# Optimization experiments

Hardware: AMD Instinct MI355X
Metric: run time of the kernel (lower is better)

## Reference

```python
import jax, jax.numpy as jnp
import numpy as np

F, P, H, HEADS, C, NCLS = 18, 128, 256, 8, 32, 625
SCALES = (2, 4, 6)
MAX_ITER = 2  # self.max_iterations in the source


def _mhsa(x, Wq, bq, Wk, bk, Wv, bv, Wo, bo):
    # x: [B, S, H]. Adjacency mask is all-ones in the source (adjacency()
    # returns torch.ones), so the mask is a mathematical no-op and is omitted.
    B, S, _ = x.shape
    hd = H // HEADS
    q = (x @ Wq + bq).reshape(B, S, HEADS, hd)
    k = (x @ Wk + bk).reshape(B, S, HEADS, hd)
    v = (x @ Wv + bv).reshape(B, S, HEADS, hd)
    scores = jnp.einsum('bqhd,bkhd->bhqk', q, k) / jnp.sqrt(jnp.float32(hd))
    attn = jax.nn.softmax(scores, axis=-1)
    out = jnp.einsum('bhqk,bkhd->bqhd', attn, v).reshape(B, S, H)
    return out @ Wo + bo


def _temporal_locality(scale, emb, Wq, bq, Wk, bk, Wv, bv, Wo, bo):
    # Vectorized overlap-add version of the python loop over windows.
    nw = F - scale + 1
    idx = jnp.arange(nw)[:, None] + jnp.arange(scale)[None, :]   # [nw, scale]
    windows = emb[idx].reshape(nw, scale * P, H)                 # [nw, s*P, H]
    out = _mhsa(windows, Wq, bq, Wk, bk, Wv, bv, Wo, bo)
    out = out.reshape(nw * scale, P, H)
    gval = jnp.zeros((F, P, H), emb.dtype).at[idx.reshape(-1)].add(out)
    # overlap counts == the hardcoded norm_scale vectors for F=18
    counts = jnp.zeros((F,), emb.dtype).at[idx.reshape(-1)].add(1.0)
    return gval / counts[:, None, None]


def _forward(multiscale_embed, unary_W, unary_b, halt_W, halt_b, compat,
             mp_W, mp_b, cls_W, cls_b,
             mhsa_Wq, mhsa_bq, mhsa_Wk, mhsa_bk,
             mhsa_Wv, mhsa_bv, mhsa_Wo, mhsa_bo):
    context = jnp.zeros_like(multiscale_embed)                 # [F, P, H]
    ptn = jnp.zeros((F,), multiscale_embed.dtype)
    Rt = jnp.zeros_like(ptn)
    Nt = jnp.zeros_like(ptn)
    # unary potentials: [F, P, C] -> permute -> [P, F, C]
    marginal = (multiscale_embed @ unary_W + unary_b).transpose(1, 0, 2)
    inputs = multiscale_embed                                   # [F, P, H]
    for _ in range(MAX_ITER):
        # --- halting probability (ACT-style) ---
        p = jnp.mean(jax.nn.sigmoid(inputs @ halt_W + halt_b), axis=1)[:, 0]  # [F]
        run = (ptn < 1.0).astype(ptn.dtype)
        new_halted = (ptn + p * run > 0.99).astype(ptn.dtype) * run
        run = (ptn + p * run <= 0.99).astype(ptn.dtype) * run
        ptn = ptn + p * run
        Rt = Rt + new_halted * (1.0 - ptn)
        ptn = ptn + new_halted * Rt
        Nt = Nt + run + new_halted
        # --- message passing: multi-scale windowed self-attention ---
        g = jnp.zeros_like(inputs)
        for i, s in enumerate(SCALES):
            g = g + _temporal_locality(s, inputs,
                                       mhsa_Wq[i], mhsa_bq[i], mhsa_Wk[i], mhsa_bk[i],
                                       mhsa_Wv[i], mhsa_bv[i], mhsa_Wo[i], mhsa_bo[i])
        temporal = 0.25 * g                                     # [F, P, H]
        inputs_p = temporal.transpose(1, 0, 2)                  # [P, F, H]
        pairwise = inputs_p @ mp_W + mp_b                       # [P, F, C]
        # compatibility transform: the chunk/cat reshuffle is an identity
        # permutation; the math is out_k = sum_c compat[k,c] * pairwise[...,c]
        pairwise = jnp.einsum('pfc,kc->pfk', pairwise, compat)
        marginal = marginal - pairwise
        # --- transition function ---
        w = (p * run + new_halted * Rt)[:, None, None]          # [F,1,1]
        inputs = inputs_p.transpose(1, 0, 2)                    # [F, P, H]
        context = inputs * w + context * (1.0 - w)
    # --- cluster features ---
    # chunk/cat flattening uses index order p*F + f on both tensors
    m = jax.nn.softmax(marginal, axis=2).reshape(P * F, C)
    ctx = context.transpose(1, 0, 2).reshape(P * F, H)
    cluster_features = m.T @ ctx                                # [C, H]
    classes = jnp.sum(cluster_features, axis=0, keepdims=True) @ cls_W + cls_b
    return classes                                              # [1, NCLS]


def setup_inputs() -> dict:
    key = jax.random.key(0)
    ks = jax.random.split(key, 16)
    init = lambda k, shape: jax.random.normal(k, shape, dtype=jnp.float32) * 0.02
    return {
        'multiscale_embed': jax.random.normal(ks[0], (F, P, H), dtype=jnp.float32),
        'unary_W': init(ks[1], (H, C)),
        'unary_b': jnp.zeros((C,), jnp.float32),
        'halt_W': init(ks[2], (H, 1)),
        'halt_b': jnp.ones((1,), jnp.float32),  # bias filled with 1.0 in source
        'compat': -jnp.eye(C, dtype=jnp.float32),
        'mp_W': init(ks[3], (H, C)),
        'mp_b': jnp.zeros((C,), jnp.float32),
        'cls_W': init(ks[4], (H, NCLS)),
        'cls_b': jnp.zeros((NCLS,), jnp.float32),
        'mhsa_Wq': init(ks[5], (3, H, H)),
        'mhsa_bq': jnp.zeros((3, H), jnp.float32),
        'mhsa_Wk': init(ks[6], (3, H, H)),
        'mhsa_bk': jnp.zeros((3, H), jnp.float32),
        'mhsa_Wv': init(ks[7], (3, H, H)),
        'mhsa_bv': jnp.zeros((3, H), jnp.float32),
        'mhsa_Wo': init(ks[8], (3, H, H)),
        'mhsa_bo': jnp.zeros((3, H), jnp.float32),
        'labels': jax.random.randint(ks[9], (1,), 0, NCLS),
    }


def reference(multiscale_embed, unary_W, unary_b, halt_W, halt_b, compat,
              mp_W, mp_b, cls_W, cls_b,
              mhsa_Wq, mhsa_bq, mhsa_Wk, mhsa_bk,
              mhsa_Wv, mhsa_bv, mhsa_Wo, mhsa_bo, labels):
    del labels  # labels are not used in the forward math shown in the source
    return _forward(multiscale_embed, unary_W, unary_b, halt_W, halt_b, compat,
                    mp_W, mp_b, cls_W, cls_b,
                    mhsa_Wq, mhsa_bq, mhsa_Wk, mhsa_bk,
                    mhsa_Wv, mhsa_bv, mhsa_Wo, mhsa_bo)
```

## Files before the change

### kernel.cpp

```cpp
#include <hip/hip_runtime.h>
#include <hip/hip_bf16.h>

typedef __hip_bfloat16 bf16;

#define F 18
#define P 128
#define H 256
#define HEADS 8
#define HD 32
#define NCLS 625
#define FPH (F*P*H)
#define RPS 589824
#define NT16 144

#define OF_PTN    16
#define OF_RT     48
#define OF_W      80
#define OF_OSUM   128
#define OF_CTX    512
#define OF_FW     (OF_CTX + FPH)
#define WO2_HALTW 0
#define WO2_HALTB 256
#define WO2_CLSB  272
#define WO2_CLSW  912
#define WO2_BQ    160912
#define WO2_BK    161680
#define WO2_BV    162448
#define WO2_BO    163216
#define FW_TOTAL  163984
#define NF_TOTAL  (OF_FW + FW_TOTAL)

#define BB_WQT 0
#define BB_WKT 196608
#define BB_WVT 393216
#define BB_WOT 589824
#define BB_INP 786432
#define BB_QB  1376256
#define BB_KB  (BB_QB + 3*RPS)
#define BB_VT  (BB_KB + 3*RPS)
#define BB_AO  (BB_VT + 3*RPS)

typedef __attribute__((ext_vector_type(8))) short s8v;
typedef __attribute__((ext_vector_type(4))) short s4v;
typedef __attribute__((ext_vector_type(4))) float f4v;

__device__ __forceinline__ float b2f(bf16 x){ return __bfloat162float(x); }
__device__ __forceinline__ unsigned short f2bu(float x){
    union { __hip_bfloat16 h; unsigned short u; } cv; cv.h = __float2bfloat16(x); return cv.u;
}
__device__ __forceinline__ float bu2f(unsigned short u){
    union { unsigned int x; float f; } cv; cv.x = ((unsigned int)u) << 16; return cv.f;
}
__device__ __forceinline__ void b2x2(unsigned int u, float& a, float& b){
    union { unsigned int x; float f; } c1, c2;
    c1.x = u << 16; c2.x = u & 0xffff0000u; a = c1.f; b = c2.f;
}

#if __has_builtin(__builtin_amdgcn_cvt_pk_bf16_f32)
typedef __attribute__((ext_vector_type(2))) __bf16 bf2_t;
__device__ __forceinline__ unsigned int pk2(float a, float b){
    union { bf2_t v; unsigned int u; } cv;
    cv.v = __builtin_amdgcn_cvt_pk_bf16_f32(a, b);
    return cv.u;
}
#else
__device__ __forceinline__ unsigned int pk2(float a, float b){
    return (unsigned int)f2bu(a) | ((unsigned int)f2bu(b) << 16);
}
#endif

#if __has_builtin(__builtin_amdgcn_exp2f)
__device__ __forceinline__ float fexp2(float x){ return __builtin_amdgcn_exp2f(x); }
#else
__device__ __forceinline__ float fexp2(float x){ return exp2f(x); }
#endif

__device__ __forceinline__ int imin(int a,int b){ return a<b?a:b; }
__device__ __forceinline__ int imax(int a,int b){ return a>b?a:b; }

__device__ __forceinline__ int detect_bf16_block(const unsigned int* __restrict__ embw,
                                                 int* scnt)
{
    if (threadIdx.x == 0) *scnt = 0;
    __syncthreads();
    int c = 0;
    {
        unsigned int e = (embw[2*threadIdx.x] >> 7) & 0xffu;
        if (e >= 120u && e <= 130u) c++;
        e = (embw[2*threadIdx.x + 1] >> 7) & 0xffu;
        if (e >= 120u && e <= 130u) c++;
    }
    atomicAdd(scnt, c);
    __syncthreads();
    return (*scnt > 256) ? 1 : 0;
}

struct ConvArgs {
    const void* src[13];
    int mode[13];
    int n[13];
    int off[13];
};
__global__ __launch_bounds__(256) void k_convert(ConvArgs a,
        const unsigned int* __restrict__ embw,
        float* __restrict__ ws, bf16* __restrict__ bb)
{
    __shared__ int scnt;
    const int isbf = detect_bf16_block(embw, &scnt);
    int gid = blockIdx.x*256 + threadIdx.x;
#pragma unroll
    for (int t = 0; t < 13; ++t){
        if (gid < a.n[t]){
            float v = isbf ? b2f(((const bf16*)a.src[t])[gid])
                           : ((const float*)a.src[t])[gid];
            if (a.mode[t] == 0){
                ws[a.off[t] + gid] = v;
            } else if (a.mode[t] == 1){
                const int i = gid >> 16, rem = gid & 65535;
                const int k = rem >> 8, nn = rem & 255;
                bb[a.off[t] + (i << 16) + (nn << 8) + k] = __float2bfloat16(v);
            } else {
                bb[BB_INP + gid] = __float2bfloat16(v);
            }
            return;
        }
        gid -= a.n[t];
    }
}

__global__ __launch_bounds__(256) void k_qkv_mfma(const bf16* __restrict__ X,
        const bf16* __restrict__ WQT, const bf16* __restrict__ WKT,
        const bf16* __restrict__ WVT, const float* __restrict__ fw,
        bf16* __restrict__ qball, bf16* __restrict__ kball, bf16* __restrict__ vball)
{
    const int tid = threadIdx.x;
    if (blockIdx.z == 3){
        if (blockIdx.x >= F || blockIdx.y != 0) return;
        __shared__ float hw[H];
        __shared__ float red[256];
        float* ws = (float*)fw - OF_FW;
        const float* hW = fw + WO2_HALTW;
        const int f = blockIdx.x;
        hw[tid] = hW[tid];
        __syncthreads();
        float sg = 0.f;
        if (tid < P){
            const uint4* row = (const uint4*)(X + (size_t)(f*P + tid)*H);
            float acc = fw[WO2_HALTB];
#pragma unroll
            for (int i = 0; i < 16; ++i){
                const uint4 u = row[i];
                float a0,a1,a2,a3,a4,a5,a6,a7;
                b2x2(u.x,a0,a1); b2x2(u.y,a2,a3); b2x2(u.z,a4,a5); b2x2(u.w,a6,a7);
                const int b = i*16;
                acc = fmaf(a0,hw[b+0],acc); acc = fmaf(a1,hw[b+1],acc);
                acc = fmaf(a2,hw[b+2],acc); acc = fmaf(a3,hw[b+3],acc);
                acc = fmaf(a4,hw[b+4],acc); acc = fmaf(a5,hw[b+5],acc);
                acc = fmaf(a6,hw[b+6],acc); acc = fmaf(a7,hw[b+7],acc);
            }
            sg = 1.f/(1.f + __expf(-acc));
        }
        red[tid] = sg;
        __syncthreads();
        for (int s = 128; s > 0; s >>= 1){ if (tid < s) red[tid] += red[tid+s]; __syncthreads(); }
        if (tid == 0){
            float pf = red[0] * (1.f/P);
            float pt = ws[OF_PTN + f], rt = ws[OF_RT + f];
            float run  = (pt < 1.f) ? 1.f : 0.f;
            float cond = (pt + pf*run > 0.99f) ? 1.f : 0.f;
            float nh   = cond*run;
            run = (1.f - cond)*run;
            pt += pf*run;
            rt += nh*(1.f - pt);
            pt += nh*rt;
            ws[OF_PTN + f] = pt; ws[OF_RT + f] = rt;
            ws[OF_W   + f] = pf*run + nh*rt;
        }
        return;
    }
    const int wave = tid >> 6, lane = tid & 63;
    const int lq = lane & 15, quad = lane >> 4;
    const int m0 = blockIdx.x * 64;
    const int n0 = blockIdx.y * 64 + wave * 16;
    const int i  = blockIdx.z;
    const int wo = i << 16;

    const bf16* arow[4];
#pragma unroll
    for (int mt = 0; mt < 4; ++mt)
        arow[mt] = X + (size_t)(m0 + mt*16 + lq)*H + quad*8;
    const bf16* bqp = WQT + wo + (size_t)(n0 + lq)*H + quad*8;
    const bf16* bkp = WKT + wo + (size_t)(n0 + lq)*H + quad*8;
    const bf16* bvp = WVT + wo + (size_t)(n0 + lq)*H + quad*8;

    f4v aq[4], ak[4], av[4];
#pragma unroll
    for (int mt = 0; mt < 4; ++mt){
        aq[mt] = (f4v){0.f,0.f,0.f,0.f};
        ak[mt] = (f4v){0.f,0.f,0.f,0.f};
        av[mt] = (f4v){0.f,0.f,0.f,0.f};
    }
#pragma unroll
    for (int k0 = 0; k0 < H; k0 += 32){
        const s8v bfq = *(const s8v*)(bqp + k0);
        const s8v bfk = *(const s8v*)(bkp + k0);
        const s8v bfv = *(const s8v*)(bvp + k0);
#pragma unroll
        for (int mt = 0; mt < 4; ++mt){
            const s8v af = *(const s8v*)(arow[mt] + k0);
            aq[mt] = __builtin_amdgcn_mfma_f32_16x16x32_bf16(bfq, af, aq[mt], 0, 0, 0);
            ak[mt] = __builtin_amdgcn_mfma_f32_16x16x32_bf16(bfk, af, ak[mt], 0, 0, 0);
            av[mt] = __builtin_amdgcn_mfma_f32_16x16x32_bf16(af, bfv, av[mt], 0, 0, 0);
        }
    }
    bf16* qo = qball + (size_t)i*RPS;
    bf16* ko = kball + (size_t)i*RPS;
    bf16* vo = vball + (size_t)i*RPS;

    const int cbase = n0 + 4*quad;
    const float4 bq4 = *(const float4*)(fw + WO2_BQ + i*256 + cbase);
    const float4 bk4 = *(const float4*)(fw + WO2_BK + i*256 + cbase);
    const int h2q  = cbase >> 5;
    const int dimq = (cbase >> 3) & 3;
    const int j2b  = cbase & 7;
    const int colv = n0 + lq;
    const float bvv = fw[WO2_BV + i*256 + colv];
    const int h2v = colv >> 5;
    const int half = (colv >> 4) & 1;
    const int lqv  = colv & 15;
#pragma unroll
    for (int mt = 0; mt < 4; ++mt){
        const int t16 = (m0 >> 4) + mt;
        const size_t qkidx = ((size_t)(h2q*NT16 + t16)*64 + lq + 16*dimq)*8 + j2b;
        uint2 qst, kst;
        qst.x = pk2(aq[mt][0] + bq4.x, aq[mt][1] + bq4.y);
        qst.y = pk2(aq[mt][2] + bq4.z, aq[mt][3] + bq4.w);
        kst.x = pk2(ak[mt][0] + bk4.x, ak[mt][1] + bk4.y);
        kst.y = pk2(ak[mt][2] + bk4.z, ak[mt][3] + bk4.w);
        *(uint2*)(qo + qkidx) = qst;
        *(uint2*)(ko + qkidx) = kst;
        const size_t vbase = ((size_t)(h2v*NT16 + t16)*64 + lqv + 16*quad)*8 + half*4;
        uint2 vst;
        vst.x = pk2(av[mt][0] + bvv, av[mt][1] + bvv);
        vst.y = pk2(av[mt][2] + bvv, av[mt][3] + bvv);
        *(uint2*)(vo + vbase) = vst;
    }
}

#if __has_builtin(__builtin_amdgcn_mfma_f32_16x16x16bf16_1k)
#define ATTN_HAVE_1K 1
#else
#define ATTN_HAVE_1K 0
#endif

template<int SS>
__device__ __forceinline__ void attn_body(const bf16* __restrict__ qs,
        const bf16* __restrict__ ks, const bf16* __restrict__ vs,
        bf16* __restrict__ aos, int f, int h, int t, int lane)
{
    const int NW = F - SS + 1;
    const int lq = lane & 15, quad = lane >> 4;
    const int qt16 = f*8 + t;

    s8v qf;
    {
        const float SCL2 = 0.17677669529663687f * 1.4426950408889634f;
        union { s8v v; unsigned int u[4]; } qin, qsc;
        qin.v = *(const s8v*)(qs + ((size_t)(h*NT16 + qt16)*64 + lane)*8);
#pragma unroll
        for (int j = 0; j < 4; ++j){
            float a, b;
            b2x2(qin.u[j], a, b);
            qsc.u[j] = pk2(a*SCL2, b*SCL2);
        }
        qf = qsc.v;
    }

    const int wLo = imax(0, f - SS + 1);
    const int wHi = imin(NW - 1, f);
    const int cnt = wHi - wLo + 1;
    const int gHi = wHi + SS - 1;

    float mw[SS], lw[SS];
    f4v ow0[SS], ow1[SS];
#pragma unroll
    for (int ws = 0; ws < SS; ++ws){
        mw[ws] = -3e38f; lw[ws] = 0.f;
        ow0[ws] = (f4v){0.f,0.f,0.f,0.f};
        ow1[ws] = (f4v){0.f,0.f,0.f,0.f};
    }

    for (int g = wLo; g <= gHi; ++g){
        const int kt0 = g*8;
        f4v st[8];
#pragma unroll
        for (int tt = 0; tt < 4; ++tt){
            const s8v kf0 = *(const s8v*)(ks + ((size_t)(h*NT16 + kt0 + tt*2    )*64 + lane)*8);
            const s8v kf1 = *(const s8v*)(ks + ((size_t)(h*NT16 + kt0 + tt*2 + 1)*64 + lane)*8);
            f4v z = {0.f,0.f,0.f,0.f};
            st[2*tt]   = __builtin_amdgcn_mfma_f32_16x16x32_bf16(kf0, qf, z, 0, 0, 0);
            st[2*tt+1] = __builtin_amdgcn_mfma_f32_16x16x32_bf16(kf1, qf, z, 0, 0, 0);
        }
        union { uint4 q; s4v h2v[2]; } vA[4], vB[4];
#pragma unroll
        for (int tt = 0; tt < 4; ++tt){
            vA[tt].q = *(const uint4*)(vs + ((size_t)(h*NT16 + kt0 + tt*2    )*64 + lane)*8);
            vB[tt].q = *(const uint4*)(vs + ((size_t)(h*NT16 + kt0 + tt*2 + 1)*64 + lane)*8);
        }
        float mu = -3e38f;
#pragma unroll
        for (int t8 = 0; t8 < 8; ++t8)
            mu = fmaxf(mu, fmaxf(fmaxf(st[t8][0], st[t8][1]), fmaxf(st[t8][2], st[t8][3])));
        mu = fmaxf(mu, __shfl_xor(mu, 16));
        mu = fmaxf(mu, __shfl_xor(mu, 32));
        float Lg = 0.f;
#pragma unroll
        for (int t8 = 0; t8 < 8; ++t8){
#pragma unroll
            for (int r = 0; r < 4; ++r){
                const float e = fexp2(st[t8][r] - mu);
                st[t8][r] = e;
                Lg += e;
            }
        }
        Lg += __shfl_xor(Lg, 16);
        Lg += __shfl_xor(Lg, 32);
        f4v P0 = {0.f,0.f,0.f,0.f}, P1 = {0.f,0.f,0.f,0.f};
#pragma unroll
        for (int tt = 0; tt < 4; ++tt){
#if ATTN_HAVE_1K
            union { unsigned int u[2]; s4v v; } pf0, pf1;
            pf0.u[0] = pk2(st[2*tt][0],   st[2*tt][1]);
            pf0.u[1] = pk2(st[2*tt][2],   st[2*tt][3]);
            pf1.u[0] = pk2(st[2*tt+1][0], st[2*tt+1][1]);
            pf1.u[1] = pk2(st[2*tt+1][2], st[2*tt+1][3]);
            P0 = __builtin_amdgcn_mfma_f32_16x16x16bf16_1k(vA[tt].h2v[0], pf0.v, P0, 0, 0, 0);
            P0 = __builtin_amdgcn_mfma_f32_16x16x16bf16_1k(vB[tt].h2v[0], pf1.v, P0, 0, 0, 0);
            P1 = __builtin_amdgcn_mfma_f32_16x16x16bf16_1k(vA[tt].h2v[1], pf0.v, P1, 0, 0, 0);
            P1 = __builtin_amdgcn_mfma_f32_16x16x16bf16_1k(vB[tt].h2v[1], pf1.v, P1, 0, 0, 0);
#else
            union { s4v h2v[2]; s8v v; } va0, va1;
            va0.h2v[0] = vA[tt].h2v[0]; va0.h2v[1] = vB[tt].h2v[0];
            va1.h2v[0] = vA[tt].h2v[1]; va1.h2v[1] = vB[tt].h2v[1];
            const unsigned int p0x = pk2(st[2*tt][0],   st[2*tt][1]);
            const unsigned int p0y = pk2(st[2*tt][2],   st[2*tt][3]);
            const unsigned int p1x = pk2(st[2*tt+1][0], st[2*tt+1][1]);
            const unsigned int p1y = pk2(st[2*tt+1][2], st[2*tt+1][3]);
            const int srcA = lq + ((( quad<<1)      & 3) << 4);
            const int srcB = lq + ((((quad<<1) | 1) & 3) << 4);
            const unsigned int a0 = (unsigned int)__shfl((int)p0x, srcA);
            const unsigned int a1 = (unsigned int)__shfl((int)p0y, srcA);
            const unsigned int a2 = (unsigned int)__shfl((int)p0x, srcB);
            const unsigned int a3 = (unsigned int)__shfl((int)p0y, srcB);
            const unsigned int b0 = (unsigned int)__shfl((int)p1x, srcA);
            const unsigned int b1 = (unsigned int)__shfl((int)p1y, srcA);
            const unsigned int b2 = (unsigned int)__shfl((int)p1x, srcB);
            const unsigned int b3 = (unsigned int)__shfl((int)p1y, srcB);
            const bool hi = (quad >= 2);
            union { unsigned int u[4]; s8v v; } bfr;
            bfr.u[0] = hi ? b0 : a0; bfr.u[1] = hi ? b1 : a1;
            bfr.u[2] = hi ? b2 : a2; bfr.u[3] = hi ? b3 : a3;
            P0 = __builtin_amdgcn_mfma_f32_16x16x32_bf16(va0.v, bfr.v, P0, 0, 0, 0);
            P1 = __builtin_amdgcn_mfma_f32_16x16x32_bf16(va1.v, bfr.v, P1, 0, 0, 0);
#endif
        }
#pragma unroll
        for (int ws = 0; ws < SS; ++ws){
            const int w = wLo + ws;
            if (w <= wHi && w <= g && w >= g - SS + 1){
                const float mn = fmaxf(mw[ws], mu);
                const float a = fexp2(mw[ws] - mn);
                const float b = fexp2(mu - mn);
                lw[ws] = lw[ws]*a + Lg*b;
#pragma unroll
                for (int r = 0; r < 4; ++r){
                    ow0[ws][r] = ow0[ws][r]*a + P0[r]*b;
                    ow1[ws][r] = ow1[ws][r]*a + P1[r]*b;
                }
                mw[ws] = mn;
            }
        }
    }
    f4v acc0 = {0.f,0.f,0.f,0.f}, acc1 = {0.f,0.f,0.f,0.f};
#pragma unroll
    for (int ws = 0; ws < SS; ++ws){
        if (ws < cnt){
            const float inv = 1.f / (lw[ws] * (float)cnt);
#pragma unroll
            for (int r = 0; r < 4; ++r){
                acc0[r] += ow0[ws][r]*inv;
                acc1[r] += ow1[ws][r]*inv;
            }
        }
    }
    const int grp0 = (4*h + (quad >> 1)) & 3;
    const int grp1 = (4*h + 2 + (quad >> 1)) & 3;
    const int off  = 4*(quad & 1);
    const size_t base = (size_t)(qt16*8 + h)*64;
    uint2 s0, s1;
    s0.x = pk2(acc0[0], acc0[1]); s0.y = pk2(acc0[2], acc0[3]);
    s1.x = pk2(acc1[0], acc1[1]); s1.y = pk2(acc1[2], acc1[3]);
    *(uint2*)(aos + (base + lq + 16*grp0)*8 + off) = s0;
    *(uint2*)(aos + (base + lq + 16*grp1)*8 + off) = s1;
}

__global__ __launch_bounds__(256) void k_attn_fused(const bf16* __restrict__ qball,
        const bf16* __restrict__ kball, const bf16* __restrict__ vball,
        bf16* __restrict__ aoall)
{
    const int bid = blockIdx.x;
    int i, rel;
    if (bid < 288)      { i = 2; rel = bid; }
    else if (bid < 576) { i = 1; rel = bid - 288; }
    else                { i = 0; rel = bid - 576; }
    const int f = rel >> 4;
    const int rest = rel & 15;
    const int h = rest >> 1;
    const int wave = threadIdx.x >> 6, lane = threadIdx.x & 63;
    const int t = (rest & 1)*4 + wave;

    const bf16* qs = qball + (size_t)i*RPS;
    const bf16* ks = kball + (size_t)i*RPS;
    const bf16* vs = vball + (size_t)i*RPS;
    bf16* aos = aoall + (size_t)i*RPS;

    if (i == 2)      attn_body<6>(qs, ks, vs, aos, f, h, t, lane);
    else if (i == 1) attn_body<4>(qs, ks, vs, aos, f, h, t, lane);
    else             attn_body<2>(qs, ks, vs, aos, f, h, t, lane);
}

__global__ __launch_bounds__(256) void k_oproj_trans(const bf16* __restrict__ aoall,
        const bf16* __restrict__ WOT, const float* __restrict__ ws,
        bf16* __restrict__ inpb, float* __restrict__ context)
{
    const int tid = threadIdx.x;
    const int wave = tid >> 6, lane = tid & 63;
    const int lq = lane & 15, quad = lane >> 4;
    const int m0 = blockIdx.x * 64;
    const int n0 = blockIdx.y * 64 + wave * 16;

    f4v acc[4];
#pragma unroll
    for (int mt = 0; mt < 4; ++mt) acc[mt] = (f4v){0.f,0.f,0.f,0.f};

    for (int i = 0; i < 3; ++i){
        const bf16* A = aoall + (size_t)i*RPS;
        const bf16* bp = WOT + (i<<16) + (size_t)(n0 + lq)*H + quad*8;
#pragma unroll
        for (int k0 = 0; k0 < H; k0 += 32){
            const s8v bf_ = *(const s8v*)(bp + k0);
#pragma unroll
            for (int mt = 0; mt < 4; ++mt){
                const s8v af = *(const s8v*)(A +
                    ((size_t)(((m0 >> 4) + mt)*8 + (k0 >> 5))*64 + lane)*8);
                acc[mt] = __builtin_amdgcn_mfma_f32_16x16x32_bf16(af, bf_, acc[mt], 0, 0, 0);
            }
        }
    }
    const int col = n0 + lq;
    const float bosum = ws[OF_FW + WO2_BO + col] + ws[OF_FW + WO2_BO + 256 + col]
                      + ws[OF_FW + WO2_BO + 512 + col];
#pragma unroll
    for (int mt = 0; mt < 4; ++mt){
#pragma unroll
        for (int r = 0; r < 4; ++r){
            const int row = m0 + mt*16 + quad*4 + r;
            const float tval = 0.25f * (acc[mt][r] + bosum);
            const float wf = ws[OF_W + (row >> 7)];
            const size_t idx = (size_t)row*H + col;
            inpb[idx] = __float2bfloat16(tval);
            context[idx] = tval*wf + context[idx]*(1.f - wf);
        }
    }
}

__global__ __launch_bounds__(256) void k_reduce(const float* __restrict__ context,
        float* __restrict__ osum)
{
    const int hcol = threadIdx.x;
    const float* base = context + (size_t)blockIdx.x * 64 * H;
    float s = 0.f;
#pragma unroll 8
    for (int r = 0; r < 64; ++r) s += base[(size_t)r*H + hcol];
    atomicAdd(&osum[hcol], s);
}

__global__ __launch_bounds__(256) void k_classes(const float* __restrict__ ws,
        const unsigned int* __restrict__ embw, void* __restrict__ out)
{
    __shared__ int scnt;
    __shared__ float os[H];
    const int isbf = detect_bf16_block(embw, &scnt);
    const int tid = threadIdx.x;
    os[tid] = ws[OF_OSUM + tid];
    __syncthreads();
    const int n = blockIdx.x*256 + tid;
    if (n < NCLS){
        const float* clsW = ws + OF_FW + WO2_CLSW;
        float acc = ws[OF_FW + WO2_CLSB + n];
        for (int hh = 0; hh < H; ++hh) acc = fmaf(os[hh], clsW[(size_t)hh*NCLS + n], acc);
        if (isbf) ((bf16*)out)[n] = __float2bfloat16(acc);
        else      ((float*)out)[n] = acc;
    }
}

extern "C" void kernel_launch(void* const* d_in, const int* in_sizes, int n_in,
                              void* d_out, int out_size, void* d_ws, size_t ws_size,
                              hipStream_t stream)
{
    (void)in_sizes; (void)n_in; (void)out_size; (void)ws_size;
    float* WS = (float*)d_ws;
    float* context = WS + OF_CTX;
    float* fw      = WS + OF_FW;
    bf16*  bb      = (bf16*)(WS + NF_TOTAL);
    bf16*  inpb    = bb + BB_INP;
    bf16*  qb      = bb + BB_QB;
    bf16*  kb      = bb + BB_KB;
    bf16*  vT      = bb + BB_VT;
    bf16*  ao      = bb + BB_AO;

    (void)hipMemsetAsync(WS, 0, (size_t)OF_FW*4, stream);

    ConvArgs ca;
    const int srcs[13]  = {0, 3, 4, 8, 9, 11, 13, 15, 17, 10, 12, 14, 16};
    const int modes[13] = {2, 0, 0, 0, 0, 0, 0, 0, 0, 1, 1, 1, 1};
    const int ns[13]    = {FPH, 256, 1, H*NCLS, NCLS, 768, 768, 768, 768,
                           196608, 196608, 196608, 196608};
    const int offs[13]  = {0,
        OF_FW+WO2_HALTW, OF_FW+WO2_HALTB, OF_FW+WO2_CLSW, OF_FW+WO2_CLSB,
        OF_FW+WO2_BQ, OF_FW+WO2_BK, OF_FW+WO2_BV, OF_FW+WO2_BO,
        BB_WQT, BB_WKT, BB_WVT, BB_WOT};
    int total = 0;
    for (int t = 0; t < 13; ++t){
        ca.src[t] = d_in[srcs[t]]; ca.mode[t] = modes[t];
        ca.n[t] = ns[t]; ca.off[t] = offs[t]; total += ns[t];
    }
    k_convert<<<(total + 255)/256, 256, 0, stream>>>(ca,
        (const unsigned int*)d_in[0], WS, bb);

    for (int it = 0; it < 2; ++it){
        k_qkv_mfma<<<dim3(36, 4, 4), 256, 0, stream>>>(inpb,
            bb+BB_WQT, bb+BB_WKT, bb+BB_WVT, fw, qb, kb, vT);
        k_attn_fused<<<864, 256, 0, stream>>>(qb, kb, vT, ao);
        k_oproj_trans<<<dim3(36, 4), 256, 0, stream>>>(ao, bb+BB_WOT, WS,
            inpb, context);
    }
    k_reduce<<<36, 256, 0, stream>>>(context, WS + OF_OSUM);
    k_classes<<<3, 256, 0, stream>>>(WS, (const unsigned int*)d_in[0], d_out);
}
```

Before: 227.1 us.

## Share one running max across windows in attention and fold memset into convert

The fused attention kernel now keeps a single running max shared by all overlapping windows instead of one per window. The accumulators are rescaled only when the max grows, which removes two exp2 calls per window per key group. The workspace memset is folded into the convert kernel, saving one launch. The classifier kernel now reads cls_W and cls_b straight from the raw inputs, so the large cls_W copy in the convert kernel goes away. A shared max stays exact for softmax but can lose precision if one window's scores sit far below the max.

```diff
diff --git a/kernel.cpp b/kernel.cpp
--- a/kernel.cpp
+++ b/kernel.cpp
@@ -21,13 +21,11 @@
 #define OF_FW     (OF_CTX + FPH)
 #define WO2_HALTW 0
 #define WO2_HALTB 256
-#define WO2_CLSB  272
-#define WO2_CLSW  912
-#define WO2_BQ    160912
-#define WO2_BK    161680
-#define WO2_BV    162448
-#define WO2_BO    163216
-#define FW_TOTAL  163984
+#define WO2_BQ    272
+#define WO2_BK    1040
+#define WO2_BV    1808
+#define WO2_BO    2576
+#define FW_TOTAL  3344
 #define NF_TOTAL  (OF_FW + FW_TOTAL)
 
 #define BB_WQT 0
@@ -96,10 +94,10 @@
 }
 
 struct ConvArgs {
-    const void* src[13];
-    int mode[13];
-    int n[13];
-    int off[13];
+    const void* src[11];
+    int mode[11];
+    int n[11];
+    int off[11];
 };
 __global__ __launch_bounds__(256) void k_convert(ConvArgs a,
         const unsigned int* __restrict__ embw,
@@ -108,8 +106,9 @@
     __shared__ int scnt;
     const int isbf = detect_bf16_block(embw, &scnt);
     int gid = blockIdx.x*256 + threadIdx.x;
-#pragma unroll
-    for (int t = 0; t < 13; ++t){
+    if (gid < OF_FW) ws[gid] = 0.f;
+#pragma unroll
+    for (int t = 0; t < 11; ++t){
         if (gid < a.n[t]){
             float v = isbf ? b2f(((const bf16*)a.src[t])[gid])
                            : ((const float*)a.src[t])[gid];
@@ -281,11 +280,12 @@
     const int cnt = wHi - wLo + 1;
     const int gHi = wHi + SS - 1;
 
-    float mw[SS], lw[SS];
+    float m = -3e38f;
+    float lw[SS];
     f4v ow0[SS], ow1[SS];
 #pragma unroll
     for (int ws = 0; ws < SS; ++ws){
-        mw[ws] = -3e38f; lw[ws] = 0.f;
+        lw[ws] = 0.f;
         ow0[ws] = (f4v){0.f,0.f,0.f,0.f};
         ow1[ws] = (f4v){0.f,0.f,0.f,0.f};
     }
@@ -364,20 +364,31 @@
             P1 = __builtin_amdgcn_mfma_f32_16x16x32_bf16(va1.v, bfr.v, P1, 0, 0, 0);
 #endif
         }
+        float b;
+        if (mu > m){
+            const float al = fexp2(m - mu);
+#pragma unroll
+            for (int ws = 0; ws < SS; ++ws){
+                lw[ws] *= al;
+#pragma unroll
+                for (int r = 0; r < 4; ++r){ ow0[ws][r] *= al; ow1[ws][r] *= al; }
+            }
+            m = mu;
+            b = 1.f;
+        } else {
+            b = fexp2(mu - m);
+        }
+        const float Lgb = Lg * b;
 #pragma unroll
         for (int ws = 0; ws < SS; ++ws){
             const int w = wLo + ws;
             if (w <= wHi && w <= g && w >= g - SS + 1){
-                const float mn = fmaxf(mw[ws], mu);
-                const float a = fexp2(mw[ws] - mn);
-                const float b = fexp2(mu - mn);
-                lw[ws] = lw[ws]*a + Lg*b;
+                lw[ws] += Lgb;
 #pragma unroll
                 for (int r = 0; r < 4; ++r){
-                    ow0[ws][r] = ow0[ws][r]*a + P0[r]*b;
-                    ow1[ws][r] = ow1[ws][r]*a + P1[r]*b;
+                    ow0[ws][r] = fmaf(P0[r], b, ow0[ws][r]);
+                    ow1[ws][r] = fmaf(P1[r], b, ow1[ws][r]);
                 }
-                mw[ws] = mn;
             }
         }
     }
@@ -486,7 +497,9 @@
 }
 
 __global__ __launch_bounds__(256) void k_classes(const float* __restrict__ ws,
-        const unsigned int* __restrict__ embw, void* __restrict__ out)
+        const unsigned int* __restrict__ embw,
+        const void* __restrict__ clsW_raw, const void* __restrict__ clsb_raw,
+        void* __restrict__ out)
 {
     __shared__ int scnt;
     __shared__ float os[H];
@@ -496,9 +509,17 @@
     __syncthreads();
     const int n = blockIdx.x*256 + tid;
     if (n < NCLS){
-        const float* clsW = ws + OF_FW + WO2_CLSW;
-        float acc = ws[OF_FW + WO2_CLSB + n];
-        for (int hh = 0; hh < H; ++hh) acc = fmaf(os[hh], clsW[(size_t)hh*NCLS + n], acc);
+        float acc = isbf ? b2f(((const bf16*)clsb_raw)[n])
+                         : ((const float*)clsb_raw)[n];
+        if (isbf){
+            const bf16* cw = (const bf16*)clsW_raw;
+            for (int hh = 0; hh < H; ++hh)
+                acc = fmaf(os[hh], b2f(cw[(size_t)hh*NCLS + n]), acc);
+        } else {
+            const float* cw = (const float*)clsW_raw;
+            for (int hh = 0; hh < H; ++hh)
+                acc = fmaf(os[hh], cw[(size_t)hh*NCLS + n], acc);
+        }
         if (isbf) ((bf16*)out)[n] = __float2bfloat16(acc);
         else      ((float*)out)[n] = acc;
     }
@@ -519,23 +540,22 @@
     bf16*  vT      = bb + BB_VT;
     bf16*  ao      = bb + BB_AO;
 
-    (void)hipMemsetAsync(WS, 0, (size_t)OF_FW*4, stream);
-
     ConvArgs ca;
-    const int srcs[13]  = {0, 3, 4, 8, 9, 11, 13, 15, 17, 10, 12, 14, 16};
-    const int modes[13] = {2, 0, 0, 0, 0, 0, 0, 0, 0, 1, 1, 1, 1};
-    const int ns[13]    = {FPH, 256, 1, H*NCLS, NCLS, 768, 768, 768, 768,
+    const int srcs[11]  = {0, 3, 4, 11, 13, 15, 17, 10, 12, 14, 16};
+    const int modes[11] = {2, 0, 0, 0, 0, 0, 0, 1, 1, 1, 1};
+    const int ns[11]    = {FPH, 256, 1, 768, 768, 768, 768,
                            196608, 196608, 196608, 196608};
-    const int offs[13]  = {0,
-        OF_FW+WO2_HALTW, OF_FW+WO2_HALTB, OF_FW+WO2_CLSW, OF_FW+WO2_CLSB,
+    const int offs[11]  = {0,
+        OF_FW+WO2_HALTW, OF_FW+WO2_HALTB,
         OF_FW+WO2_BQ, OF_FW+WO2_BK, OF_FW+WO2_BV, OF_FW+WO2_BO,
         BB_WQT, BB_WKT, BB_WVT, BB_WOT};
     int total = 0;
-    for (int t = 0; t < 13; ++t){
+    for (int t = 0; t < 11; ++t){
         ca.src[t] = d_in[srcs[t]]; ca.mode[t] = modes[t];
         ca.n[t] = ns[t]; ca.off[t] = offs[t]; total += ns[t];
     }
-    k_convert<<<(total + 255)/256, 256, 0, stream>>>(ca,
+    const int gmax = (total > OF_FW) ? total : OF_FW;
+    k_convert<<<(gmax + 255)/256, 256, 0, stream>>>(ca,
         (const unsigned int*)d_in[0], WS, bb);
 
     for (int it = 0; it < 2; ++it){
@@ -546,5 +566,6 @@
             inpb, context);
     }
     k_reduce<<<36, 256, 0, stream>>>(context, WS + OF_OSUM);
-    k_classes<<<3, 256, 0, stream>>>(WS, (const unsigned int*)d_in[0], d_out);
-}
+    k_classes<<<3, 256, 0, stream>>>(WS, (const unsigned int*)d_in[0],
+        d_in[8], d_in[9], d_out);
+}
```

Result: faster. 219.2 us (-3.5%).
